# Performance work log

Measured on AMD Instinct MI355X. Metric: run time of the kernel, lower is better.

Reference implementation:

```python
import jax, jax.numpy as jnp
import numpy as np

N_CLS = 5  # number of modalities / graph nodes


def _l2norm(x, eps=1e-12):
    n = jnp.linalg.norm(x, axis=-1, keepdims=True)
    return x / jnp.maximum(n, eps)


def _bn(x, g, b, eps=1e-5):
    """BatchNorm over channel axis 1 (training-mode batch stats), x: (B, Ch, ...)."""
    axes = (0,) + tuple(range(2, x.ndim))
    m = x.mean(axis=axes, keepdims=True)
    v = x.var(axis=axes, keepdims=True)
    shp = (1, -1) + (1,) * (x.ndim - 2)
    return g.reshape(shp) * (x - m) / jnp.sqrt(v + eps) + b.reshape(shp)


def _cross_attn(y, x, wq, wk, wv):
    """ME-GraphAU-style CrossAttn over the spatial (hw) axis. y,x: (..., hw, c)."""
    q = y @ wq  # (..., hw, c/2)
    k = x @ wk
    v = x @ wv
    scale = 1.0 / jnp.sqrt(jnp.asarray(wq.shape[1], jnp.float32))
    attn = jax.nn.softmax(jnp.einsum('...qd,...kd->...qk', q, k) * scale, axis=-1)
    return jnp.einsum('...qk,...kd->...qd', attn, v)


def _gnn_layer(x, edge, U, V, A, Bm, E, bnv_g, bnv_b, bne_g, bne_b, mask_node):
    """One edge-vertex GNN update. x: (b,n,t,c), edge: (b,n*n,t,c).
    Edge e = i*n + j has end-node i, start-node j (create_e_matrix layout)."""
    b, n, t, c = x.shape
    idx_i = jnp.repeat(jnp.arange(n), n)  # 'end' one-hot gather
    idx_j = jnp.tile(jnp.arange(n), n)    # 'start' one-hot gather
    res = x
    Vix = x @ A
    Vjx = x @ Bm
    e = edge @ E
    edge1 = Vix[:, idx_i] + Vjx[:, idx_j] + e  # einsum('ev,bvtc->betc') as gather
    edge1 = _bn(edge1, bne_g, bne_b)
    edge1 = jnp.where(jnp.isnan(edge1), 0.0, edge1)
    edge = edge + jax.nn.relu(edge1)
    eg = jax.nn.sigmoid(edge).reshape(b, n, n, t, c)
    eg = jax.nn.softmax(eg, axis=2).reshape(b, n * n, t, c)  # softmax over start nodes j
    Ujx = (x @ V)[:, idx_j]
    # einsum('ve,betc->bvtc', end.T, e*Ujx): scatter-sum edges to their end node i
    agg = (eg * Ujx).reshape(b, n, n, t, c).sum(axis=2) / n
    xn = x @ U + agg
    x1 = _bn(xn, bnv_g, bnv_b)
    if mask_node:
        x1 = jnp.where(jnp.isnan(x1), 0.0, x1)
    x = jax.nn.relu(res + x1)
    return x, edge


def _forward(af, ef, gf, attf, sf,
             fam_q, fam_k, fam_v, arm_q, arm_k, arm_v,
             edge_proj_w, edge_proj_b, gem_bn_g, gem_bn_b,
             U1, V1, A1, B1, E1, U2, V2, A2, B2, E2,
             bnv1_g, bnv1_b, bne1_g, bne1_b, bnv2_g, bnv2_b, bne2_g, bne2_b,
             sc, edge_fc_w, edge_fc_b):
    b, c, t, h, w = af.shape
    hw = h * w
    n = N_CLS

    def prep(f):  # (b,c,t,h,w) -> (b,t,hw,c)
        return f.reshape(b, c, t, hw).transpose(0, 2, 3, 1)

    mods = [prep(f) for f in (af, ef, gf, attf, sf)]
    f_u = jnp.stack(mods, axis=1)           # (b, 5, t, hw, c)
    f_v = f_u.mean(axis=-2)                 # (b, 5, t, c)

    # --- GEM edge extractor (ME-GraphAU style, adapted to the extra t axis) ---
    gfeat = jnp.broadcast_to(mods[0][:, None], f_u.shape)  # global feature = af
    feat = _cross_attn(f_u, gfeat, fam_q, fam_k, fam_v)    # FAM
    idx_i = jnp.repeat(jnp.arange(n), n)
    idx_j = jnp.tile(jnp.arange(n), n)
    feat_end = feat[:, idx_i]               # (b, 25, t, hw, c)
    feat_start = feat[:, idx_j]
    feat = _cross_attn(feat_start, feat_end, arm_q, arm_k, arm_v)  # ARM
    edge = feat @ edge_proj_w + edge_proj_b
    edge = _bn(edge.reshape(b, n * n, t * hw, c), gem_bn_g, gem_bn_b)
    f_e = edge.reshape(b, n * n, t, hw, c).mean(axis=-2)   # (b, 25, t, c)

    # --- 2-layer edge-vertex GNN ---
    f_v, f_e = _gnn_layer(f_v, f_e, U1, V1, A1, B1, E1,
                          bnv1_g, bnv1_b, bne1_g, bne1_b, mask_node=True)
    f_v, f_e = _gnn_layer(f_v, f_e, U2, V2, A2, B2, E2,
                          bnv2_g, bnv2_b, bne2_g, bne2_b, mask_node=False)

    # --- cosine-similarity head ---
    scn = _l2norm(jax.nn.relu(sc))                         # (5, c)
    cl = (_l2norm(f_v) * scn[None, :, None, :]).sum(axis=-1)  # (b, 5, t)
    cl_edge = jnp.einsum('bntc,c->bnt', f_e, edge_fc_w)[..., None] + edge_fc_b  # (b,25,t,1)
    return cl, cl_edge


def setup_inputs() -> dict:
    B, C, T, H, W = 8, 256, 16, 7, 7
    key = jax.random.key(0)
    ks = jax.random.split(key, 40)
    d = {}
    for i, name in enumerate(['af', 'ef', 'gf', 'attf', 'sf']):
        d[name] = jax.random.normal(ks[i], (B, C, T, H, W), jnp.float32)
    gs = float(np.sqrt(2.0 / C))   # GNN linear init scale
    xs = float(np.sqrt(2.0 / (2 * C)))  # xavier-like
    k = 5
    def nrm(shape, s):
        nonlocal k
        k += 1
        return jax.random.normal(ks[k], shape, jnp.float32) * s
    d['fam_q'] = nrm((C, C // 2), xs); d['fam_k'] = nrm((C, C // 2), xs); d['fam_v'] = nrm((C, C), xs)
    d['arm_q'] = nrm((C, C // 2), xs); d['arm_k'] = nrm((C, C // 2), xs); d['arm_v'] = nrm((C, C), xs)
    d['edge_proj_w'] = nrm((C, C), xs); d['edge_proj_b'] = jnp.zeros((C,), jnp.float32)
    d['gem_bn_g'] = jnp.ones((N_CLS * N_CLS,), jnp.float32); d['gem_bn_b'] = jnp.zeros((N_CLS * N_CLS,), jnp.float32)
    for nm in ['U1', 'V1', 'A1', 'B1', 'E1', 'U2', 'V2', 'A2', 'B2', 'E2']:
        d[nm] = nrm((C, C), gs)
    for nm, sz in [('bnv1', N_CLS), ('bne1', N_CLS * N_CLS), ('bnv2', N_CLS), ('bne2', N_CLS * N_CLS)]:
        d[nm + '_g'] = jnp.ones((sz,), jnp.float32)
        d[nm + '_b'] = jnp.zeros((sz,), jnp.float32)
    d['sc'] = nrm((N_CLS, C), xs)
    d['edge_fc_w'] = nrm((C,), xs)
    d['edge_fc_b'] = jnp.zeros((1,), jnp.float32)
    return d


def reference(af, ef, gf, attf, sf,
              fam_q, fam_k, fam_v, arm_q, arm_k, arm_v,
              edge_proj_w, edge_proj_b, gem_bn_g, gem_bn_b,
              U1, V1, A1, B1, E1, U2, V2, A2, B2, E2,
              bnv1_g, bnv1_b, bne1_g, bne1_b, bnv2_g, bnv2_b, bne2_g, bne2_b,
              sc, edge_fc_w, edge_fc_b):
    return _forward(af, ef, gf, attf, sf,
                    fam_q, fam_k, fam_v, arm_q, arm_k, arm_v,
                    edge_proj_w, edge_proj_b, gem_bn_g, gem_bn_b,
                    U1, V1, A1, B1, E1, U2, V2, A2, B2, E2,
                    bnv1_g, bnv1_b, bne1_g, bne1_b, bnv2_g, bnv2_b, bne2_g, bne2_b,
                    sc, edge_fc_w, edge_fc_b)
```

## Files before the change

### kernel.cpp

```cpp
#include <hip/hip_runtime.h>

#define DEV __device__ __forceinline__

typedef unsigned short bhalf;
typedef __attribute__((ext_vector_type(8))) short bf8v;
typedef __attribute__((ext_vector_type(4))) float f4;
typedef __attribute__((ext_vector_type(4))) unsigned short us4;

namespace {
constexpr int TPB = 256;
constexpr float ATT_SCALE = 0.08838834764831845f;

constexpr size_t O_PT  = 0;
constexpr size_t O_WTS = 20971520;
constexpr size_t O_K1B = 21626880;
constexpr size_t O_FW  = 23724032;
constexpr size_t O_VQT = 27918336;
constexpr size_t O_VKT = 30015488;
constexpr size_t O_G   = 32112640;
constexpr size_t O_VWT = 36306944;
constexpr size_t O_Q2B = 40501248;
constexpr size_t O_K2B = 50987008;
constexpr size_t O_W2T = 61472768;
constexpr size_t O_FV  = 82444288;
constexpr size_t O_HWS = 83099648;
constexpr size_t O_EDG = 86376448;
constexpr size_t O_XA  = 89654272;
constexpr size_t O_XB  = 90309632;
constexpr size_t O_XU  = 90964992;
constexpr size_t O_XV  = 91620352;
constexpr size_t O_EE  = 92275712;
constexpr size_t O_ET  = 95552512;
constexpr size_t O_XN  = 98829312;
constexpr size_t O_GWT = 99484672;
constexpr size_t O_CSE = 100795392;
constexpr size_t O_FVB = 100796416;
constexpr size_t O_HWB = 101124096;
constexpr size_t O_EDB = 102762496;

constexpr size_t W_FAMQ = 0, W_FAMK = 32768, W_ARMQ = 65536, W_ARMK = 98304,
                 W_FAMV = 131072, W_ARMV = 196608, W_EPW = 262144;
constexpr size_t FW_VQ = 0, FW_VK = 32768, FW_VW = 65536;

constexpr int ST_GS1 = 0, ST_GS2 = 256;
}


DEV bhalf f2b(float f) {
  unsigned u = __float_as_uint(f);
  return (bhalf)((u + 0x7FFFu + ((u >> 16) & 1u)) >> 16);
}

DEV f4 mfma16(bf8v a, bf8v b, f4 c) {
  return __builtin_amdgcn_mfma_f32_16x16x32_bf16(a, b, c, 0, 0, 0);
}

DEV bf8v ldfrag(const bhalf* base, int r0, int k0, int S, int l) {
  return *reinterpret_cast<const bf8v*>(base + (size_t)(r0 + (l & 15)) * S + k0 + ((l >> 4) << 3));
}

DEV bf8v ldswz(const bhalf* base, int row, int koffB, int strideB) {
  int byte = row * strideB + koffB;
  byte ^= ((row & 7) << 4);
  return *reinterpret_cast<const bf8v*>(reinterpret_cast<const char*>(base) + byte);
}

DEV float sumShards(const float* base, int idx) {
  float s = 0.f;
  #pragma unroll
  for (int x = 0; x < 8; ++x) s += base[x*32 + idx];
  return s;
}

DEV void regSoftmax(float sv[4][4]) {
  #pragma unroll
  for (int reg = 0; reg < 4; ++reg) {
    float m = fmaxf(fmaxf(sv[0][reg], sv[1][reg]), fmaxf(sv[2][reg], sv[3][reg]));
    #pragma unroll
    for (int off = 1; off <= 8; off <<= 1) m = fmaxf(m, __shfl_xor(m, off));
    float s = 0.f;
    #pragma unroll
    for (int nt = 0; nt < 4; ++nt) { float e = __expf(sv[nt][reg] - m); sv[nt][reg] = e; s += e; }
    #pragma unroll
    for (int off = 1; off <= 8; off <<= 1) s += __shfl_xor(s, off);
    float inv = 1.f / s;
    #pragma unroll
    for (int nt = 0; nt < 4; ++nt) sv[nt][reg] *= inv;
  }
}

DEV void reduce2Atomic(float a, float b, float* ga, float* gb, float* red) {
  #pragma unroll
  for (int off = 32; off; off >>= 1) { a += __shfl_down(a, off); b += __shfl_down(b, off); }
  if ((threadIdx.x & 63) == 0) { int w = threadIdx.x >> 6; red[w*2] = a; red[w*2+1] = b; }
  __syncthreads();
  if (threadIdx.x == 0) {
    atomicAdd(ga, red[0]+red[2]+red[4]+red[6]);
    atomicAdd(gb, red[1]+red[3]+red[5]+red[7]);
  }
  __syncthreads();
}


__global__ void __launch_bounds__(256) prepAll(const float* fq, const float* fk, const float* fv,
                                               const float* aq, const float* ak, const float* av,
                                               const float* ep, bhalf* WT,
                                               const float* af, const float* ef, const float* gf,
                                               const float* attf, const float* sf,
                                               bhalf* PT, float* FV, float* G,
                                               const float* A1, const float* B1, const float* U1,
                                               const float* V1, const float* E1,
                                               const float* A2, const float* B2, const float* U2,
                                               const float* V2, const float* E2,
                                               bhalf* GWT, float* CSE, bhalf* FVB) {
  __shared__ float lb[49*260];
  int tid = threadIdx.x;
  if (blockIdx.x < 1280) {
    int blk = blockIdx.x;
    const float* src; bhalf* dst; int N, n;
    if (blk < 512) {
      int m = blk >> 7; n = blk & 127; N = 128;
      src = (m==0)?fq:(m==1)?fk:(m==2)?aq:ak;
      dst = WT + (size_t)m*32768;
    } else {
      int r = blk - 512; int m = r >> 8; n = r & 255; N = 256;
      src = (m==0)?fv:(m==1)?av:ep;
      dst = WT + 131072 + (size_t)m*65536;
    }
    dst[(size_t)n*256 + tid] = f2b(src[(size_t)tid*N + n]);
  } else if (blockIdx.x < 1920) {
    int blk = blockIdx.x - 1280;
    int u = blk % 5, bt = blk / 5, b = bt >> 4, t = bt & 15;
    const float* src = (u==0)?af:(u==1)?ef:(u==2)?gf:(u==3)?attf:sf;
    src += ((size_t)b*256*16 + t)*49;
    for (int o = tid; o < 49*256; o += TPB) {
      int c = o / 49, p = o % 49;
      lb[p*260 + c] = src[(size_t)c*784 + p];
    }
    __syncthreads();
    bhalf* pt = PT + (size_t)blk*16384;
    for (int p = 0; p < 64; ++p)
      pt[p*256 + tid] = (p < 49) ? f2b(lb[p*260 + tid]) : (bhalf)0;
    float s = 0.f;
    for (int p = 0; p < 49; ++p) s += lb[p*260 + tid];
    float mval = s * (1.f/49.f);
    size_t idx = (((size_t)(b*5+u)*16) + t)*256 + tid;
    FV[idx] = mval;
    FVB[idx] = f2b(mval);
  } else if (blockIdx.x < 2176) {
    int c = blockIdx.x - 1920;
    const float* ar = av + (size_t)c*256;
    float acc = 0.f;
    for (int d = 0; d < 256; ++d)
      acc = fmaf(ar[d], ep[(size_t)d*256 + tid], acc);
    G[(size_t)c*256 + tid] = acc;
  } else if (blockIdx.x < 4736) {
    int blk = blockIdx.x - 2176;
    int m = blk >> 8, n = blk & 255;
    const float* src = (m==0)?A1:(m==1)?B1:(m==2)?U1:(m==3)?V1:(m==4)?E1:
                       (m==5)?A2:(m==6)?B2:(m==7)?U2:(m==8)?V2:E2;
    GWT[(size_t)m*65536 + (size_t)n*256 + tid] = f2b(src[(size_t)tid*256 + n]);
  } else {
    float s = 0.f;
    for (int c = 0; c < 256; ++c) s += E1[(size_t)c*256 + tid];
    CSE[tid] = s;
  }
}

__global__ void __launch_bounds__(256) wf2(const float* fv, const float* aq, const float* ak,
                                           const float* G, bhalf* FW) {
  int blk = blockIdx.x, tid = threadIdx.x;
  if (blk < 256) {
    int k = blk;
    if (tid < 128) {
      float a1 = 0.f, a2 = 0.f;
      for (int c = 0; c < 256; ++c) {
        float f = fv[(size_t)k*256 + c];
        a1 = fmaf(f, aq[(size_t)c*128 + tid], a1);
        a2 = fmaf(f, ak[(size_t)c*128 + tid], a2);
      }
      FW[FW_VQ + (size_t)tid*256 + k] = f2b(a1);
      FW[FW_VK + (size_t)tid*256 + k] = f2b(a2);
    }
  } else {
    int k = blk - 256;
    float a = 0.f;
    for (int c = 0; c < 256; ++c)
      a = fmaf(fv[(size_t)k*256 + c], G[(size_t)c*256 + tid], a);
    FW[FW_VW + (size_t)tid*256 + k] = f2b(a);
  }
}

__global__ void __launch_bounds__(256, 4) kv1(const bhalf* PT, const bhalf* WT, const bhalf* FW,
                                              bhalf* K1B, bhalf* VQT, bhalf* VKT, bhalf* VWT,
                                              bhalf* Q2B) {
  __shared__ bhalf Wl[64*256];
  int bt = blockIdx.x, part = blockIdx.y;
  int tid = threadIdx.x, w = tid >> 6, l = tid & 63;
  const bhalf* Wsrc; int nt0;
  const bhalf* A;
  if (part >= 10) {
    int u = (part - 10) >> 1;
    nt0 = ((part - 10) & 1) * 4;
    Wsrc = WT + W_FAMQ;
    A = PT + (size_t)(bt*5 + u)*16384;
  } else if (part < 2) {
    nt0 = part*4; Wsrc = WT + W_FAMK; A = PT + (size_t)bt*5*16384;
  } else if (part < 6) {
    nt0 = ((part - 2) & 1) * 4;
    Wsrc = FW + (((part - 2) >> 1) == 0 ? FW_VQ : FW_VK);
    A = PT + (size_t)bt*5*16384;
  } else {
    nt0 = (part - 6)*4; Wsrc = FW + FW_VW; A = PT + (size_t)bt*5*16384;
  }
  bf8v a8[8];
  #pragma unroll
  for (int kt = 0; kt < 8; ++kt) a8[kt] = ldfrag(A, w*16, kt*32, 256, l);
  {
    const char* gw = reinterpret_cast<const char*>(Wsrc + (size_t)nt0*16*256);
    char* lw = reinterpret_cast<char*>(Wl);
    #pragma unroll
    for (int c = 0; c < 8; ++c) {
      int x = (c*256 + tid) << 4;
      float4 val = *reinterpret_cast<const float4*>(gw + x);
      *reinterpret_cast<float4*>(lw + (x ^ (((x >> 9) & 7) << 4))) = val;
    }
  }
  __syncthreads();
  __builtin_amdgcn_s_setprio(1);
  f4 accs[4];
  #pragma unroll
  for (int nn = 0; nn < 4; ++nn) {
    f4 acc = {0.f,0.f,0.f,0.f};
    #pragma unroll
    for (int kt = 0; kt < 8; ++kt)
      acc = mfma16(a8[kt], ldswz(Wl, nn*16 + (l & 15), kt*64 + ((l >> 4) << 4), 512), acc);
    accs[nn] = acc;
  }
  __builtin_amdgcn_s_setprio(0);
  if (part >= 10) {
    int u = (part - 10) >> 1;
    bhalf* q1 = Q2B + (size_t)(bt*5 + u)*8192;
    #pragma unroll
    for (int nn = 0; nn < 4; ++nn) {
      int nt = nt0 + nn;
      #pragma unroll
      for (int reg = 0; reg < 4; ++reg) {
        int p = w*16 + ((l>>4)<<2) + reg;
        q1[(size_t)p*128 + nt*16 + (l&15)] = f2b(accs[nn][reg]);
      }
    }
  } else if (part < 2) {
    bhalf* dst = K1B + (size_t)bt*8192;
    #pragma unroll
    for (int nn = 0; nn < 4; ++nn) {
      int nt = nt0 + nn;
      #pragma unroll
      for (int reg = 0; reg < 4; ++reg) {
        int p = w*16 + ((l>>4)<<2) + reg;
        dst[(size_t)p*128 + nt*16 + (l&15)] = f2b(accs[nn][reg]);
      }
    }
  } else if (part < 6) {
    bhalf* o = ((((part - 2) >> 1) == 0) ? VQT : VKT) + (size_t)bt*8192;
    #pragma unroll
    for (int nn = 0; nn < 4; ++nn) {
      int n = (nt0 + nn)*16 + (l&15);
      int p0 = w*16 + ((l>>4)<<2);
      us4 pk = { f2b(accs[nn][0]), f2b(accs[nn][1]), f2b(accs[nn][2]), f2b(accs[nn][3]) };
      *reinterpret_cast<us4*>(o + (size_t)n*64 + p0) = pk;
    }
  } else {
    bhalf* ow = VWT + (size_t)bt*16384;
    #pragma unroll
    for (int nn = 0; nn < 4; ++nn) {
      int n = (nt0 + nn)*16 + (l&15);
      int p0 = w*16 + ((l>>4)<<2);
      us4 pk = { f2b(accs[nn][0]), f2b(accs[nn][1]), f2b(accs[nn][2]), f2b(accs[nn][3]) };
      *reinterpret_cast<us4*>(ow + (size_t)n*64 + p0) = pk;
    }
  }
}

__global__ void __launch_bounds__(256) s1ker(const bhalf* WT,
    const bhalf* K1B, const bhalf* VQT, const bhalf* VKT, const bhalf* VWT,
    bhalf* Q2B, bhalf* K2B, bhalf* W2T)
{
  __shared__ bhalf bufP[64*72];
  int orig = blockIdx.x;
  int blk = (orig & 7) * 80 + (orig >> 3);
  int bt = blk / 5;
  int tid = threadIdx.x, w = tid >> 6, l = tid & 63;
  float sv[4][4];
  {
    const bhalf* Q1 = Q2B + (size_t)blk*8192;
    const bhalf* K1 = K1B + (size_t)bt*8192;
    bf8v aq[4];
    #pragma unroll
    for (int kt = 0; kt < 4; ++kt) aq[kt] = ldfrag(Q1, w*16, kt*32, 128, l);
    __builtin_amdgcn_s_setprio(1);
    #pragma unroll
    for (int nt = 0; nt < 4; ++nt) {
      f4 acc = {0.f,0.f,0.f,0.f};
      #pragma unroll
      for (int kt = 0; kt < 4; ++kt)
        acc = mfma16(aq[kt], ldfrag(K1, nt*16, kt*32, 128, l), acc);
      #pragma unroll
      for (int reg = 0; reg < 4; ++reg) sv[nt][reg] = acc[reg] * ATT_SCALE;
    }
    __builtin_amdgcn_s_setprio(0);
  }
  if ((l & 15) > 0) { sv[3][0] = -1e30f; sv[3][1] = -1e30f; sv[3][2] = -1e30f; sv[3][3] = -1e30f; }
  regSoftmax(sv);
  #pragma unroll
  for (int nt = 0; nt < 4; ++nt)
    #pragma unroll
    for (int reg = 0; reg < 4; ++reg)
      bufP[(w*16 + ((l>>4)<<2) + reg)*72 + nt*16 + (l&15)] = f2b(sv[nt][reg]);
  __syncthreads();
  bf8v ap0[4], ap1[4];
  #pragma unroll
  for (int g = 0; g < 4; ++g) {
    ap0[g] = ldfrag(bufP, g*16, 0, 72, l);
    ap1[g] = ldfrag(bufP, g*16, 32, 72, l);
  }
  const bhalf* vq = VQT + (size_t)bt*8192;
  const bhalf* vk = VKT + (size_t)bt*8192;
  const bhalf* vw = VWT + (size_t)bt*16384;
  bhalf* q2 = Q2B + (size_t)blk*8192;
  bhalf* k2 = K2B + (size_t)blk*8192;
  bhalf* w2 = W2T + (size_t)blk*16384;
  __builtin_amdgcn_s_setprio(1);
  #pragma unroll
  for (int nn = 0; nn < 2; ++nn) {
    int nt = w*2 + nn;
    bf8v b0 = ldfrag(vq, nt*16, 0, 64, l);
    bf8v b1 = ldfrag(vq, nt*16, 32, 64, l);
    f4 acc[4];
    #pragma unroll
    for (int g = 0; g < 4; ++g) {
      f4 z = {0.f,0.f,0.f,0.f};
      z = mfma16(ap0[g], b0, z);
      acc[g] = mfma16(ap1[g], b1, z);
    }
    int c = nt*16 + (l & 15);
    #pragma unroll
    for (int g = 0; g < 4; ++g)
      #pragma unroll
      for (int reg = 0; reg < 4; ++reg) {
        int p = g*16 + ((l>>4)<<2) + reg;
        q2[(size_t)p*128 + c] = (p < 49) ? f2b(acc[g][reg]) : (bhalf)0;
      }
  }
  #pragma unroll
  for (int nn = 0; nn < 2; ++nn) {
    int nt = w*2 + nn;
    bf8v b0 = ldfrag(vk, nt*16, 0, 64, l);
    bf8v b1 = ldfrag(vk, nt*16, 32, 64, l);
    f4 acc[4];
    #pragma unroll
    for (int g = 0; g < 4; ++g) {
      f4 z = {0.f,0.f,0.f,0.f};
      z = mfma16(ap0[g], b0, z);
      acc[g] = mfma16(ap1[g], b1, z);
    }
    int c = nt*16 + (l & 15);
    #pragma unroll
    for (int g = 0; g < 4; ++g)
      #pragma unroll
      for (int reg = 0; reg < 4; ++reg) {
        int p = g*16 + ((l>>4)<<2) + reg;
        k2[(size_t)p*128 + c] = (p < 49) ? f2b(acc[g][reg]) : (bhalf)0;
      }
  }
  #pragma unroll
  for (int nn = 0; nn < 4; ++nn) {
    int nt = w*4 + nn;
    bf8v b0 = ldfrag(vw, nt*16, 0, 64, l);
    bf8v b1 = ldfrag(vw, nt*16, 32, 64, l);
    f4 acc[4];
    #pragma unroll
    for (int g = 0; g < 4; ++g) {
      f4 z = {0.f,0.f,0.f,0.f};
      z = mfma16(ap0[g], b0, z);
      acc[g] = mfma16(ap1[g], b1, z);
    }
    int c = nt*16 + (l & 15);
    int p0 = (l >> 4) << 2;
    #pragma unroll
    for (int g = 0; g < 4; ++g) {
      int pb = g*16 + p0;
      us4 pk = { (bhalf)((pb+0 < 49) ? f2b(acc[g][0]) : 0),
                 (bhalf)((pb+1 < 49) ? f2b(acc[g][1]) : 0),
                 (bhalf)((pb+2 < 49) ? f2b(acc[g][2]) : 0),
                 (bhalf)((pb+3 < 49) ? f2b(acc[g][3]) : 0) };
      *reinterpret_cast<us4*>(w2 + (size_t)c*64 + pb) = pk;
    }
  }
  __builtin_amdgcn_s_setprio(0);
}

__global__ void __launch_bounds__(256) s2ker(const bhalf* Q2B, const bhalf* K2B, const bhalf* W2T,
    const float* epb, float* hws, bhalf* hwsb, float* gs1, float* gs2)
{
  __shared__ bhalf Kl[64*128];
  __shared__ bhalf bufP[64*72];
  __shared__ float redH[256];
  __shared__ float redS[8];
  int orig = blockIdx.x;
  int blk = (orig & 7) * 400 + (orig >> 3);
  int e = blk % 25, bt = blk / 25, b = bt >> 4, t = bt & 15;
  int i = e / 5, j = e % 5;
  int tid = threadIdx.x, w = tid >> 6, l = tid & 63;
  const bhalf* K = K2B + (size_t)(bt*5 + i)*8192;
  const bhalf* V = W2T + (size_t)(bt*5 + i)*16384;
  const bhalf* Q = Q2B + (size_t)(bt*5 + j)*8192;
  bf8v aq[4];
  #pragma unroll
  for (int kt = 0; kt < 4; ++kt) aq[kt] = ldfrag(Q, w*16, kt*32, 128, l);
  {
    const char* gk = reinterpret_cast<const char*>(K);
    char* lk = reinterpret_cast<char*>(Kl);
    #pragma unroll
    for (int c = 0; c < 4; ++c) {
      int x = (c*256 + tid) << 4;
      float4 val = *reinterpret_cast<const float4*>(gk + x);
      *reinterpret_cast<float4*>(lk + (x ^ (((x >> 8) & 7) << 4))) = val;
    }
  }
  __syncthreads();
  float sv[4][4];
  __builtin_amdgcn_s_setprio(1);
  #pragma unroll
  for (int nt = 0; nt < 4; ++nt) {
    f4 acc = {0.f,0.f,0.f,0.f};
    #pragma unroll
    for (int kt = 0; kt < 4; ++kt)
      acc = mfma16(aq[kt], ldswz(Kl, nt*16 + (l & 15), kt*64 + ((l >> 4) << 4), 256), acc);
    #pragma unroll
    for (int reg = 0; reg < 4; ++reg) sv[nt][reg] = acc[reg] * ATT_SCALE;
  }
  __builtin_amdgcn_s_setprio(0);
  if ((l & 15) > 0) { sv[3][0] = -1e30f; sv[3][1] = -1e30f; sv[3][2] = -1e30f; sv[3][3] = -1e30f; }
  regSoftmax(sv);
  #pragma unroll
  for (int nt = 0; nt < 4; ++nt)
    #pragma unroll
    for (int reg = 0; reg < 4; ++reg)
      bufP[(w*16 + ((l>>4)<<2) + reg)*72 + nt*16 + (l&15)] = f2b(sv[nt][reg]);
  bf8v vf0[4], vf1[4];
  #pragma unroll
  for (int nn = 0; nn < 4; ++nn) {
    vf0[nn] = ldfrag(V, (w*4 + nn)*16, 0, 64, l);
    vf1[nn] = ldfrag(V, (w*4 + nn)*16, 32, 64, l);
  }
  __syncthreads();
  bf8v ap0[4], ap1[4];
  #pragma unroll
  for (int g = 0; g < 4; ++g) {
    ap0[g] = ldfrag(bufP, g*16, 0, 72, l);
    ap1[g] = ldfrag(bufP, g*16, 32, 72, l);
  }
  float sqa = 0.f;
  __builtin_amdgcn_s_setprio(1);
  #pragma unroll
  for (int nn = 0; nn < 4; ++nn) {
    f4 acc[4];
    #pragma unroll
    for (int g = 0; g < 4; ++g) {
      f4 z = {0.f,0.f,0.f,0.f};
      z = mfma16(ap0[g], vf0[nn], z);
      acc[g] = mfma16(ap1[g], vf1[nn], z);
    }
    int c = ((w*4 + nn) << 4) + (l & 15);
    float bias = epb[c];
    float hw = 0.f;
    #pragma unroll
    for (int g = 0; g < 4; ++g) {
      #pragma unroll
      for (int reg = 0; reg < 4; ++reg) {
        int p = g*16 + ((l>>4)<<2) + reg;
        if (p < 49) { float v = acc[g][reg] + bias; hw += v; sqa += v*v; }
      }
    }
    hw += __shfl_xor(hw, 16);
    hw += __shfl_xor(hw, 32);
    if ((l >> 4) == 0) redH[c] = hw;
  }
  __builtin_amdgcn_s_setprio(0);
  __syncthreads();
  float hwtot = redH[tid];
  size_t oidx = (((size_t)(b*25+e)*16) + t)*256 + tid;
  hws[oidx] = hwtot;
  hwsb[oidx] = f2b(hwtot);
  int slot = (orig & 7)*32 + e;
  reduce2Atomic(hwtot, sqa, gs1 + slot, gs2 + slot, redS);
}


__global__ void __launch_bounds__(256, 2) gnnProjM(const bhalf* Xb, const bhalf* Eb,
    const bhalf* GW, const float* CSE,
    const float* gs1, const float* gs2, const float* gg, const float* gb, int bnfly,
    float* xA, float* xB, float* xU, float* xV, float* eE) {
  __shared__ bhalf Wl[64*256];
  int blk = blockIdx.x;
  int tid = threadIdx.x, w = tid >> 6, l = tid & 63;
  const bhalf* A; const bhalf* Wsrc; float* dst; int rt, ct, isE;
  if (blk < 160) {
    int m = blk / 40, rem = blk % 40; rt = rem >> 2; ct = rem & 3;
    A = Xb + (size_t)rt*64*256;
    Wsrc = GW + (size_t)m*65536;
    dst = (m==0)?xA:(m==1)?xB:(m==2)?xU:xV;
    isE = 0;
  } else {
    int eb = blk - 160; rt = eb >> 2; ct = eb & 3;
    A = Eb + (size_t)rt*64*256;
    Wsrc = GW + (size_t)4*65536;
    dst = eE; isE = 1;
  }
  bf8v a8[8];
  #pragma unroll
  for (int kt = 0; kt < 8; ++kt) a8[kt] = ldfrag(A, w*16, kt*32, 256, l);
  {
    const char* gw = reinterpret_cast<const char*>(Wsrc + (size_t)ct*64*256);
    char* lw = reinterpret_cast<char*>(Wl);
    #pragma unroll
    for (int c = 0; c < 8; ++c) {
      int x = (c*256 + tid) << 4;
      float4 val = *reinterpret_cast<const float4*>(gw + x);
      *reinterpret_cast<float4*>(lw + (x ^ (((x >> 9) & 7) << 4))) = val;
    }
  }
  __syncthreads();
  __builtin_amdgcn_s_setprio(1);
  f4 accs[4];
  #pragma unroll
  for (int nn = 0; nn < 4; ++nn) {
    f4 acc = {0.f,0.f,0.f,0.f};
    #pragma unroll
    for (int kt = 0; kt < 8; ++kt)
      acc = mfma16(a8[kt], ldswz(Wl, nn*16 + (l & 15), kt*64 + ((l >> 4) << 4), 512), acc);
    accs[nn] = acc;
  }
  __builtin_amdgcn_s_setprio(0);
  int p0 = w*16 + ((l>>4)<<2);
  size_t rbase = (size_t)rt*64 + p0;
  if (isE && bnfly) {
    int e = (rt*4 + w) % 25;
    constexpr float invCnt = 1.f/1605632.f;
    float m = sumShards(gs1, e)*invCnt;
    float var = sumShards(gs2, e)*invCnt - m*m;
    float rstd = rsqrtf(var + 1e-5f);
    float g = gg[e]*rstd;
    float scl = g * (1.f/49.f);
    float ofs = gb[e] - g*m;
    #pragma unroll
    for (int nn = 0; nn < 4; ++nn) {
      int n = ct*64 + nn*16 + (l&15);
      float cs = CSE[n] * ofs;
      #pragma unroll
      for (int reg = 0; reg < 4; ++reg)
        dst[(rbase + reg)*256 + n] = fmaf(accs[nn][reg], scl, cs);
    }
  } else {
    #pragma unroll
    for (int nn = 0; nn < 4; ++nn) {
      int n = ct*64 + nn*16 + (l&15);
      #pragma unroll
      for (int reg = 0; reg < 4; ++reg)
        dst[(rbase + reg)*256 + n] = accs[nn][reg];
    }
  }
}

__global__ void __launch_bounds__(256) g2a(const float* xA, const float* xB, const float* eE,
                                           float* ET, float* s1, float* s2) {
  __shared__ float red[8];
  int blk = blockIdx.x, tid = threadIdx.x;
  int b = blk / 400, e = (blk >> 4) % 25, t = blk & 15;
  int i = e / 5, j = e % 5;
  size_t ni = ((size_t)(b*5+i)*16 + t)*256 + tid;
  size_t nj = ((size_t)(b*5+j)*16 + t)*256 + tid;
  size_t ee = (size_t)blk*256 + tid;
  float v = xA[ni] + xB[nj] + eE[ee];
  ET[ee] = v;
  int slot = (blk & 7)*32 + e;
  reduce2Atomic(v, v*v, s1 + slot, s2 + slot, red);
}

__global__ void __launch_bounds__(256) g2bg3a(const float* ET, const float* HWS, const float* EDGin,
    float* EDGout, bhalf* EDGb, const float* xV, const float* xU, float* XN,
    const float* gs1, const float* gs2, const float* gemg, const float* gemb,
    const float* bg, const float* bb2, const float* es1, const float* es2,
    float* ns1, float* ns2, const float* efw, const float* efb, float* out, int layer) {
  __shared__ float red[8];
  int blk = blockIdx.x, tid = threadIdx.x;
  int b = blk / 80, i = (blk >> 4) % 5, t = blk & 15;
  constexpr float inv32k = 1.f/32768.f;
  constexpr float invCnt = 1.f/1605632.f;
  float ssum = 0.f, exv[5], xvv[5];
  #pragma unroll
  for (int j = 0; j < 5; ++j) {
    int e = i*5 + j;
    size_t ee = ((size_t)(b*25 + e)*16 + t)*256 + tid;
    float m = sumShards(es1, e)*inv32k;
    float var = sumShards(es2, e)*inv32k - m*m;
    float rstd = rsqrtf(var + 1e-5f);
    float v = bg[e]*((ET[ee]-m)*rstd) + bb2[e];
    if (v != v) v = 0.f;
    float base;
    if (layer == 0) {
      float gm = sumShards(gs1, e)*invCnt;
      float gvar = sumShards(gs2, e)*invCnt - gm*gm;
      float gr = rsqrtf(gvar + 1e-5f);
      base = gemg[e]*((HWS[ee]*(1.f/49.f) - gm)*gr) + gemb[e];
    } else {
      base = EDGin[ee];
    }
    float edg = base + fmaxf(v, 0.f);
    if (layer == 0) {
      EDGout[ee] = edg;
      EDGb[ee] = f2b(edg);
    } else {
      float vv = edg * efw[tid];
      #pragma unroll
      for (int off = 32; off; off >>= 1) vv += __shfl_down(vv, off);
      if ((tid & 63) == 0) red[tid >> 6] = vv;
      __syncthreads();
      if (tid == 0) out[640 + (size_t)(b*25 + e)*16 + t] = red[0]+red[1]+red[2]+red[3] + efb[0];
      __syncthreads();
    }
    float sg = 1.f/(1.f + __expf(-edg));
    exv[j] = __expf(sg);
    ssum += exv[j];
    xvv[j] = xV[((size_t)(b*5+j)*16 + t)*256 + tid];
  }
  float agg = 0.f;
  #pragma unroll
  for (int j = 0; j < 5; ++j) agg += exv[j]*xvv[j];
  agg *= 0.2f/ssum;
  float xn = xU[(size_t)blk*256 + tid] + agg;
  XN[(size_t)blk*256 + tid] = xn;
  int slot = (blk & 7)*32 + i;
  reduce2Atomic(xn, xn*xn, ns1 + slot, ns2 + slot, red);
}

__global__ void __launch_bounds__(256) g3b(const float* XN, float* X, bhalf* Xb,
                                           const float* g, const float* bb,
                                           const float* s1, const float* s2, int mask) {
  int blk = blockIdx.x, tid = threadIdx.x;
  int i = (blk >> 4) % 5;
  size_t ni = (size_t)blk*256 + tid;
  constexpr float invCnt = 1.f/32768.f;
  float m = sumShards(s1, i)*invCnt;
  float var = sumShards(s2, i)*invCnt - m*m;
  float rstd = rsqrtf(var + 1e-5f);
  float v = g[i]*((XN[ni]-m)*rstd) + bb[i];
  if (mask && v != v) v = 0.f;
  float nv = fmaxf(X[ni] + v, 0.f);
  X[ni] = nv;
  Xb[ni] = f2b(nv);
}

__global__ void __launch_bounds__(256) g3bfin(const float* XN, const float* FV,
    const float* g, const float* bb, const float* s1, const float* s2,
    const float* sc, float* out) {
  __shared__ float red[12];
  int blk = blockIdx.x, tid = threadIdx.x;
  int i = (blk >> 4) % 5;
  size_t ni = (size_t)blk*256 + tid;
  constexpr float inv32k = 1.f/32768.f;
  float m = sumShards(s1, i)*inv32k;
  float var = sumShards(s2, i)*inv32k - m*m;
  float rstd = rsqrtf(var + 1e-5f);
  float v = g[i]*((XN[ni]-m)*rstd) + bb[i];
  float x = fmaxf(FV[ni] + v, 0.f);
  float s = fmaxf(sc[i*256 + tid], 0.f);
  float xx = x*x, ss = s*s, xs = x*s;
  #pragma unroll
  for (int off = 32; off; off >>= 1) {
    xx += __shfl_down(xx, off); ss += __shfl_down(ss, off); xs += __shfl_down(xs, off);
  }
  if ((tid & 63) == 0) { int w = tid >> 6; red[w*3] = xx; red[w*3+1] = ss; red[w*3+2] = xs; }
  __syncthreads();
  if (tid == 0) {
    float sxx = red[0]+red[3]+red[6]+red[9];
    float sss = red[1]+red[4]+red[7]+red[10];
    float sxs = red[2]+red[5]+red[8]+red[11];
    float nx = fmaxf(sqrtf(sxx), 1e-12f);
    float ns = fmaxf(sqrtf(sss), 1e-12f);
    out[blk] = sxs / (nx * ns);
  }
}


extern "C" void kernel_launch(void* const* d_in, const int* in_sizes, int n_in,
                              void* d_out, int out_size, void* d_ws, size_t ws_size,
                              hipStream_t stream) {
  (void)in_sizes; (void)n_in; (void)out_size; (void)ws_size;
  const float* af    = (const float*)d_in[0];
  const float* ef    = (const float*)d_in[1];
  const float* gfm   = (const float*)d_in[2];
  const float* attf  = (const float*)d_in[3];
  const float* sfm   = (const float*)d_in[4];
  const float* fam_q = (const float*)d_in[5];
  const float* fam_k = (const float*)d_in[6];
  const float* fam_v = (const float*)d_in[7];
  const float* arm_q = (const float*)d_in[8];
  const float* arm_k = (const float*)d_in[9];
  const float* arm_v = (const float*)d_in[10];
  const float* epw   = (const float*)d_in[11];
  const float* epb   = (const float*)d_in[12];
  const float* gemg  = (const float*)d_in[13];
  const float* gemb  = (const float*)d_in[14];
  const float* Us[2]   = {(const float*)d_in[15], (const float*)d_in[20]};
  const float* Vs[2]   = {(const float*)d_in[16], (const float*)d_in[21]};
  const float* As[2]   = {(const float*)d_in[17], (const float*)d_in[22]};
  const float* Bs[2]   = {(const float*)d_in[18], (const float*)d_in[23]};
  const float* Es[2]   = {(const float*)d_in[19], (const float*)d_in[24]};
  const float* bnvg[2] = {(const float*)d_in[25], (const float*)d_in[29]};
  const float* bnvb[2] = {(const float*)d_in[26], (const float*)d_in[30]};
  const float* bneg[2] = {(const float*)d_in[27], (const float*)d_in[31]};
  const float* bneb[2] = {(const float*)d_in[28], (const float*)d_in[32]};
  const float* scp  = (const float*)d_in[33];
  const float* efw  = (const float*)d_in[34];
  const float* efb  = (const float*)d_in[35];

  char* ws = (char*)d_ws;
  bhalf* PT  = (bhalf*)(ws + O_PT);
  bhalf* WTS = (bhalf*)(ws + O_WTS);
  bhalf* K1B = (bhalf*)(ws + O_K1B);
  bhalf* FW  = (bhalf*)(ws + O_FW);
  bhalf* VQT = (bhalf*)(ws + O_VQT);
  bhalf* VKT = (bhalf*)(ws + O_VKT);
  float* G   = (float*)(ws + O_G);
  float* ST2 = (float*)(ws + O_G);
  bhalf* VWT = (bhalf*)(ws + O_VWT);
  bhalf* Q2B = (bhalf*)(ws + O_Q2B);
  bhalf* K2B = (bhalf*)(ws + O_K2B);
  bhalf* W2T = (bhalf*)(ws + O_W2T);
  float* FV  = (float*)(ws + O_FV);
  float* HWS = (float*)(ws + O_HWS);
  float* EDG = (float*)(ws + O_EDG);
  float* XA  = (float*)(ws + O_XA);
  float* XB  = (float*)(ws + O_XB);
  float* XU  = (float*)(ws + O_XU);
  float* XV  = (float*)(ws + O_XV);
  float* EE  = (float*)(ws + O_EE);
  float* ET  = (float*)(ws + O_ET);
  float* XN  = (float*)(ws + O_XN);
  bhalf* GWT = (bhalf*)(ws + O_GWT);
  float* CSE = (float*)(ws + O_CSE);
  bhalf* FVB = (bhalf*)(ws + O_FVB);
  bhalf* HWB = (bhalf*)(ws + O_HWB);
  bhalf* EDB = (bhalf*)(ws + O_EDB);

  prepAll<<<4737, TPB, 0, stream>>>(fam_q, fam_k, fam_v, arm_q, arm_k, arm_v, epw, WTS,
                                    af, ef, gfm, attf, sfm, PT, FV, G,
                                    As[0], Bs[0], Us[0], Vs[0], Es[0],
                                    As[1], Bs[1], Us[1], Vs[1], Es[1],
                                    GWT, CSE, FVB);
  wf2<<<512, TPB, 0, stream>>>(fam_v, arm_q, arm_k, G, FW);
  hipMemsetAsync(ST2, 0, 2560*sizeof(float), stream);
  kv1<<<dim3(128, 20), TPB, 0, stream>>>(PT, WTS, FW, K1B, VQT, VKT, VWT, Q2B);
  s1ker<<<640, TPB, 0, stream>>>(WTS, K1B, VQT, VKT, VWT, Q2B, K2B, W2T);
  s2ker<<<3200, TPB, 0, stream>>>(Q2B, K2B, W2T, epb, HWS, HWB, ST2 + ST_GS1, ST2 + ST_GS2);

  float* out = (float*)d_out;
  for (int L = 0; L < 2; ++L) {
    float* es1 = ST2 + 512 + L*1024;
    float* es2 = ST2 + 768 + L*1024;
    float* ns1 = ST2 + 1024 + L*1024;
    float* ns2 = ST2 + 1280 + L*1024;
    gnnProjM<<<360, TPB, 0, stream>>>(FVB, (L == 0) ? HWB : EDB,
                                      GWT + (size_t)L*5*65536, CSE,
                                      ST2 + ST_GS1, ST2 + ST_GS2, gemg, gemb, (L == 0) ? 1 : 0,
                                      XA, XB, XU, XV, EE);
    g2a<<<3200, TPB, 0, stream>>>(XA, XB, EE, ET, es1, es2);
    g2bg3a<<<640, TPB, 0, stream>>>(ET, HWS, EDG, EDG, EDB, XV, XU, XN,
                                    ST2 + ST_GS1, ST2 + ST_GS2, gemg, gemb,
                                    bneg[L], bneb[L], es1, es2, ns1, ns2,
                                    efw, efb, out, L);
    if (L == 0)
      g3b<<<640, TPB, 0, stream>>>(XN, FV, FVB, bnvg[0], bnvb[0], ns1, ns2, 1);
    else
      g3bfin<<<640, TPB, 0, stream>>>(XN, FV, bnvg[1], bnvb[1], ns1, ns2, scp, out);
  }
}
```

Measured before the change: 167.8 us.

## Fuse edge projection with edge gather-add and BN statistics, split node projection

```diff
diff --git a/kernel.cpp b/kernel.cpp
--- a/kernel.cpp
+++ b/kernel.cpp
@@ -498,26 +498,15 @@
 }
 
 
-__global__ void __launch_bounds__(256, 2) gnnProjM(const bhalf* Xb, const bhalf* Eb,
-    const bhalf* GW, const float* CSE,
-    const float* gs1, const float* gs2, const float* gg, const float* gb, int bnfly,
-    float* xA, float* xB, float* xU, float* xV, float* eE) {
+__global__ void __launch_bounds__(256, 2) gnnProjN(const bhalf* Xb, const bhalf* GW,
+    float* xA, float* xB, float* xU, float* xV) {
   __shared__ bhalf Wl[64*256];
   int blk = blockIdx.x;
   int tid = threadIdx.x, w = tid >> 6, l = tid & 63;
-  const bhalf* A; const bhalf* Wsrc; float* dst; int rt, ct, isE;
-  if (blk < 160) {
-    int m = blk / 40, rem = blk % 40; rt = rem >> 2; ct = rem & 3;
-    A = Xb + (size_t)rt*64*256;
-    Wsrc = GW + (size_t)m*65536;
-    dst = (m==0)?xA:(m==1)?xB:(m==2)?xU:xV;
-    isE = 0;
-  } else {
-    int eb = blk - 160; rt = eb >> 2; ct = eb & 3;
-    A = Eb + (size_t)rt*64*256;
-    Wsrc = GW + (size_t)4*65536;
-    dst = eE; isE = 1;
-  }
+  int m = blk / 40, rem = blk % 40, rt = rem >> 2, ct = rem & 3;
+  const bhalf* A = Xb + (size_t)rt*64*256;
+  const bhalf* Wsrc = GW + (size_t)m*65536;
+  float* dst = (m==0)?xA:(m==1)?xB:(m==2)?xU:xV;
   bf8v a8[8];
   #pragma unroll
   for (int kt = 0; kt < 8; ++kt) a8[kt] = ldfrag(A, w*16, kt*32, 256, l);
@@ -545,47 +534,85 @@
   __builtin_amdgcn_s_setprio(0);
   int p0 = w*16 + ((l>>4)<<2);
   size_t rbase = (size_t)rt*64 + p0;
-  if (isE && bnfly) {
-    int e = (rt*4 + w) % 25;
+  #pragma unroll
+  for (int nn = 0; nn < 4; ++nn) {
+    int n = ct*64 + nn*16 + (l&15);
+    #pragma unroll
+    for (int reg = 0; reg < 4; ++reg)
+      dst[(rbase + reg)*256 + n] = accs[nn][reg];
+  }
+}
+
+__global__ void __launch_bounds__(256, 2) gnnProjE(const bhalf* Eb, const bhalf* GW,
+    const float* CSE, const float* gs1, const float* gs2, const float* gg, const float* gb,
+    int bnfly, const float* xA, const float* xB, float* ET, float* es1, float* es2) {
+  __shared__ bhalf Wl[64*256];
+  int blk = blockIdx.x;
+  int tid = threadIdx.x, w = tid >> 6, l = tid & 63;
+  int rt = blk >> 2, ct = blk & 3;
+  const bhalf* A = Eb + (size_t)rt*64*256;
+  bf8v a8[8];
+  #pragma unroll
+  for (int kt = 0; kt < 8; ++kt) a8[kt] = ldfrag(A, w*16, kt*32, 256, l);
+  {
+    const char* gw = reinterpret_cast<const char*>(GW + (size_t)ct*64*256);
+    char* lw = reinterpret_cast<char*>(Wl);
+    #pragma unroll
+    for (int c = 0; c < 8; ++c) {
+      int x = (c*256 + tid) << 4;
+      float4 val = *reinterpret_cast<const float4*>(gw + x);
+      *reinterpret_cast<float4*>(lw + (x ^ (((x >> 9) & 7) << 4))) = val;
+    }
+  }
+  __syncthreads();
+  __builtin_amdgcn_s_setprio(1);
+  f4 accs[4];
+  #pragma unroll
+  for (int nn = 0; nn < 4; ++nn) {
+    f4 acc = {0.f,0.f,0.f,0.f};
+    #pragma unroll
+    for (int kt = 0; kt < 8; ++kt)
+      acc = mfma16(a8[kt], ldswz(Wl, nn*16 + (l & 15), kt*64 + ((l >> 4) << 4), 512), acc);
+    accs[nn] = acc;
+  }
+  __builtin_amdgcn_s_setprio(0);
+  int be = rt*4 + w;
+  int b = be / 25, e = be % 25;
+  int i = e / 5, j = e % 5;
+  const float* xAr = xA + ((size_t)(b*5+i)*16)*256;
+  const float* xBr = xB + ((size_t)(b*5+j)*16)*256;
+  float scl = 1.f, ofs = 0.f;
+  if (bnfly) {
     constexpr float invCnt = 1.f/1605632.f;
     float m = sumShards(gs1, e)*invCnt;
     float var = sumShards(gs2, e)*invCnt - m*m;
     float rstd = rsqrtf(var + 1e-5f);
     float g = gg[e]*rstd;
-    float scl = g * (1.f/49.f);
-    float ofs = gb[e] - g*m;
-    #pragma unroll
-    for (int nn = 0; nn < 4; ++nn) {
-      int n = ct*64 + nn*16 + (l&15);
-      float cs = CSE[n] * ofs;
-      #pragma unroll
-      for (int reg = 0; reg < 4; ++reg)
-        dst[(rbase + reg)*256 + n] = fmaf(accs[nn][reg], scl, cs);
-    }
-  } else {
-    #pragma unroll
-    for (int nn = 0; nn < 4; ++nn) {
-      int n = ct*64 + nn*16 + (l&15);
-      #pragma unroll
-      for (int reg = 0; reg < 4; ++reg)
-        dst[(rbase + reg)*256 + n] = accs[nn][reg];
-    }
-  }
-}
-
-__global__ void __launch_bounds__(256) g2a(const float* xA, const float* xB, const float* eE,
-                                           float* ET, float* s1, float* s2) {
-  __shared__ float red[8];
-  int blk = blockIdx.x, tid = threadIdx.x;
-  int b = blk / 400, e = (blk >> 4) % 25, t = blk & 15;
-  int i = e / 5, j = e % 5;
-  size_t ni = ((size_t)(b*5+i)*16 + t)*256 + tid;
-  size_t nj = ((size_t)(b*5+j)*16 + t)*256 + tid;
-  size_t ee = (size_t)blk*256 + tid;
-  float v = xA[ni] + xB[nj] + eE[ee];
-  ET[ee] = v;
-  int slot = (blk & 7)*32 + e;
-  reduce2Atomic(v, v*v, s1 + slot, s2 + slot, red);
+    scl = g * (1.f/49.f);
+    ofs = gb[e] - g*m;
+  }
+  int t0 = (l>>4)<<2;
+  float s1l = 0.f, s2l = 0.f;
+  #pragma unroll
+  for (int nn = 0; nn < 4; ++nn) {
+    int n = ct*64 + nn*16 + (l&15);
+    float cs = CSE[n] * ofs;
+    #pragma unroll
+    for (int reg = 0; reg < 4; ++reg) {
+      int t = t0 + reg;
+      float ve = fmaf(accs[nn][reg], scl, cs);
+      float vfull = xAr[(size_t)t*256 + n] + xBr[(size_t)t*256 + n] + ve;
+      ET[((size_t)be*16 + t)*256 + n] = vfull;
+      s1l += vfull; s2l += vfull*vfull;
+    }
+  }
+  #pragma unroll
+  for (int off = 32; off; off >>= 1) { s1l += __shfl_down(s1l, off); s2l += __shfl_down(s2l, off); }
+  if (l == 0) {
+    int slot = (blk & 7)*32 + e;
+    atomicAdd(es1 + slot, s1l);
+    atomicAdd(es2 + slot, s2l);
+  }
 }
 
 __global__ void __launch_bounds__(256) g2bg3a(const float* ET, const float* HWS, const float* EDGin,
@@ -746,7 +773,6 @@
   float* XB  = (float*)(ws + O_XB);
   float* XU  = (float*)(ws + O_XU);
   float* XV  = (float*)(ws + O_XV);
-  float* EE  = (float*)(ws + O_EE);
   float* ET  = (float*)(ws + O_ET);
   float* XN  = (float*)(ws + O_XN);
   bhalf* GWT = (bhalf*)(ws + O_GWT);
@@ -772,11 +798,11 @@
     float* es2 = ST2 + 768 + L*1024;
     float* ns1 = ST2 + 1024 + L*1024;
     float* ns2 = ST2 + 1280 + L*1024;
-    gnnProjM<<<360, TPB, 0, stream>>>(FVB, (L == 0) ? HWB : EDB,
-                                      GWT + (size_t)L*5*65536, CSE,
+    gnnProjN<<<160, TPB, 0, stream>>>(FVB, GWT + (size_t)L*5*65536, XA, XB, XU, XV);
+    gnnProjE<<<200, TPB, 0, stream>>>((L == 0) ? HWB : EDB,
+                                      GWT + (size_t)L*5*65536 + (size_t)4*65536, CSE,
                                       ST2 + ST_GS1, ST2 + ST_GS2, gemg, gemb, (L == 0) ? 1 : 0,
-                                      XA, XB, XU, XV, EE);
-    g2a<<<3200, TPB, 0, stream>>>(XA, XB, EE, ET, es1, es2);
+                                      XA, XB, ET, es1, es2);
     g2bg3a<<<640, TPB, 0, stream>>>(ET, HWS, EDG, EDG, EDB, XV, XU, XN,
                                     ST2 + ST_GS1, ST2 + ST_GS2, gemg, gemb,
                                     bneg[L], bneb[L], es1, es2, ns1, ns2,
```

After: 165.6 us (median of 2 runs). Within noise of the previous version (-1.3%).
